# Performance work log

Measured on AMD Instinct MI355X. Metric: run time of the kernel, lower is better.

## Reference

```python
import jax, jax.numpy as jnp
import numpy as np

IN_F, HID_F, OUT_F = 2048, 8192, 2048
BATCH = 4096

def setup_inputs() -> dict:
    key = jax.random.key(0)
    k_x, k_w1, k_b1, k_w2, k_b2 = jax.random.split(key, 5)
    # PyTorch Linear default init: U(-1/sqrt(fan_in), 1/sqrt(fan_in))
    s1 = 1.0 / np.sqrt(IN_F)
    s2 = 1.0 / np.sqrt(HID_F)
    return {
        "x":  jax.random.normal(k_x, (BATCH, IN_F), dtype=jnp.float32),
        "W1": jax.random.uniform(k_w1, (IN_F, HID_F), jnp.float32, -s1, s1),
        "b1": jax.random.uniform(k_b1, (HID_F,), jnp.float32, -s1, s1),
        "W2": jax.random.uniform(k_w2, (HID_F, OUT_F), jnp.float32, -s2, s2),
        "b2": jax.random.uniform(k_b2, (OUT_F,), jnp.float32, -s2, s2),
    }

def reference(x, W1, b1, W2, b2):
    # linear1 -> ReLU -> linear2 -> sigmoid (the original's numpy "black box"
    # is mathematically 1/(1+exp(-x)), done here on-device).
    h = jax.nn.relu(x @ W1 + b1)          # [B, hidden]
    z = h @ W2 + b2                        # [B, out]
    return jax.nn.sigmoid(z)
```

## Files before the change

kernel.cpp:

```cpp
#include <hip/hip_runtime.h>
#include <hip/hip_bf16.h>
#include <stdint.h>

#define IN_F  2048
#define HID_F 8192
#define OUT_F 2048
#define BATCH 4096

typedef __attribute__((ext_vector_type(8))) short bf16x8;
typedef __attribute__((ext_vector_type(4))) float f32x4;
typedef __attribute__((ext_vector_type(8))) unsigned short u16x8;

__device__ __forceinline__ unsigned short f32_to_bf16(float f) {
  union { float f; uint32_t u; } v; v.f = f;
  uint32_t u = v.u;
  uint32_t r = u + 0x7FFF + ((u >> 16) & 1);
  return (unsigned short)(r >> 16);
}

__device__ __forceinline__ void stage16(const unsigned short* g, unsigned short* l) {
  __builtin_amdgcn_global_load_lds(
      (const __attribute__((address_space(1))) void*)g,
      (__attribute__((address_space(3))) void*)l, 16, 0, 0);
}


__global__ void cvt_f32_bf16(const float* __restrict__ in, unsigned short* __restrict__ out, int n4) {
  int i = blockIdx.x * blockDim.x + threadIdx.x;
  int stride = gridDim.x * blockDim.x;
  for (int idx = i; idx < n4; idx += stride) {
    float4 v = ((const float4*)in)[idx];
    ushort4 o;
    o.x = f32_to_bf16(v.x); o.y = f32_to_bf16(v.y);
    o.z = f32_to_bf16(v.z); o.w = f32_to_bf16(v.w);
    ((ushort4*)out)[idx] = o;
  }
}

__global__ void transpose_cvt(const float* __restrict__ in, unsigned short* __restrict__ out,
                              int R, int C) {
  __shared__ unsigned short t[64][72];
  const int tid = threadIdx.x;
  const int r0 = blockIdx.y * 64;
  const int c0 = blockIdx.x * 64;
  #pragma unroll
  for (int p = 0; p < 4; ++p) {
    int f4  = p * 256 + tid;
    int row = f4 >> 4;
    int c   = (f4 & 15) * 4;
    float4 v = *(const float4*)&in[(size_t)(r0 + row) * C + c0 + c];
    t[c + 0][row] = f32_to_bf16(v.x);
    t[c + 1][row] = f32_to_bf16(v.y);
    t[c + 2][row] = f32_to_bf16(v.z);
    t[c + 3][row] = f32_to_bf16(v.w);
  }
  __syncthreads();
  #pragma unroll
  for (int p = 0; p < 2; ++p) {
    int u  = p * 256 + tid;
    int cc = u >> 3;
    int rr = (u & 7) * 8;
    *(u16x8*)&out[(size_t)(c0 + cc) * R + r0 + rr] = *(const u16x8*)&t[cc][rr];
  }
}

template <int EPI>
__global__ __launch_bounds__(512, 2)
void gemm_bt(const unsigned short* __restrict__ A, const unsigned short* __restrict__ Bt,
             const float* __restrict__ bias, void* __restrict__ C,
             int M, int N, int K) {
  __shared__ unsigned short lA[3][128 * 64];
  __shared__ unsigned short lB[3][256 * 64];

  const int tid  = threadIdx.x;
  const int lane = tid & 63;
  const int wave = tid >> 6;
  const int wr = wave >> 2;
  const int wc = wave & 3;

  const int nbx = N >> 8;
  const int nwg = (M >> 7) * nbx;
  int wg = blockIdx.x;
  wg = (wg & 7) * (nwg >> 3) + (wg >> 3);
  const int brow = wg / nbx;
  const int bcol = wg % nbx;

  const int srow = tid >> 3;
  const int w8   = (tid & 7) * 8;
  const unsigned short* gA[2];
  const unsigned short* gB[4];
  #pragma unroll
  for (int c = 0; c < 2; ++c) {
    int row = c * 64 + srow;
    gA[c] = A + (size_t)(brow * 128 + row) * K + (w8 ^ ((row & 7) << 3));
  }
  #pragma unroll
  for (int c = 0; c < 4; ++c) {
    int row = c * 64 + srow;
    gB[c] = Bt + (size_t)(bcol * 256 + row) * K + (w8 ^ ((row & 7) << 3));
  }
  const int ldst = tid * 8;

  const int ktiles = K >> 6;

  #pragma unroll
  for (int c = 0; c < 2; ++c) stage16(gA[c],      &lA[0][c * 4096 + ldst]);
  #pragma unroll
  for (int c = 0; c < 4; ++c) stage16(gB[c],      &lB[0][c * 4096 + ldst]);
  #pragma unroll
  for (int c = 0; c < 2; ++c) stage16(gA[c] + 64, &lA[1][c * 4096 + ldst]);
  #pragma unroll
  for (int c = 0; c < 4; ++c) stage16(gB[c] + 64, &lB[1][c * 4096 + ldst]);
  #pragma unroll
  for (int c = 0; c < 2; ++c) gA[c] += 128;
  #pragma unroll
  for (int c = 0; c < 4; ++c) gB[c] += 128;

  asm volatile("s_waitcnt vmcnt(6)" ::: "memory");
  __builtin_amdgcn_s_barrier();

  f32x4 acc[4][4] = {};
  const int fr = lane & 15;
  const int fk = (lane >> 4) * 8;

  int slot = 0;
  for (int jt = 0; jt < ktiles; ++jt) {
    const int nslot = (slot + 2 >= 3) ? slot - 1 : slot + 2;
    const bool pf = (jt + 2 < ktiles);

    #pragma unroll
    for (int kk = 0; kk < 2; ++kk) {
      bf16x8 af[4], bf[4];
      #pragma unroll
      for (int m = 0; m < 4; ++m) {
        int row = wr * 64 + m * 16 + fr;
        af[m] = *(const bf16x8*)&lA[slot][row * 64 + ((kk * 32 + fk) ^ ((row & 7) << 3))];
      }
      #pragma unroll
      for (int n = 0; n < 4; ++n) {
        int row = wc * 64 + n * 16 + fr;
        bf[n] = *(const bf16x8*)&lB[slot][row * 64 + ((kk * 32 + fk) ^ ((row & 7) << 3))];
      }
      if (pf) {
        if (kk == 0) {
          stage16(gA[0], &lA[nslot][0 * 4096 + ldst]);
          stage16(gA[1], &lA[nslot][1 * 4096 + ldst]);
          stage16(gB[0], &lB[nslot][0 * 4096 + ldst]);
        } else {
          stage16(gB[1], &lB[nslot][1 * 4096 + ldst]);
          stage16(gB[2], &lB[nslot][2 * 4096 + ldst]);
          stage16(gB[3], &lB[nslot][3 * 4096 + ldst]);
        }
      }
      __builtin_amdgcn_s_barrier();
      asm volatile("s_waitcnt lgkmcnt(0)" ::: "memory");
      __builtin_amdgcn_s_setprio(1);
      #pragma unroll
      for (int m = 0; m < 4; ++m)
        #pragma unroll
        for (int n = 0; n < 4; ++n)
          acc[m][n] = __builtin_amdgcn_mfma_f32_16x16x32_bf16(af[m], bf[n], acc[m][n], 0, 0, 0);
      __builtin_amdgcn_s_setprio(0);
      __builtin_amdgcn_s_barrier();
    }

    if (pf) {
      #pragma unroll
      for (int c = 0; c < 2; ++c) gA[c] += 64;
      #pragma unroll
      for (int c = 0; c < 4; ++c) gB[c] += 64;
    }
    if (jt + 1 < ktiles) {
      if (pf) asm volatile("s_waitcnt vmcnt(6)" ::: "memory");
      else    asm volatile("s_waitcnt vmcnt(0)" ::: "memory");
      __builtin_amdgcn_s_barrier();
    }
    slot = (slot + 1 >= 3) ? 0 : slot + 1;
  }

  const int crow0 = brow * 128 + wr * 64 + (lane >> 4) * 4;
  const int ccol0 = bcol * 256 + wc * 64 + fr;
  #pragma unroll
  for (int n = 0; n < 4; ++n) {
    const int col = ccol0 + n * 16;
    const float bv = bias[col];
    #pragma unroll
    for (int m = 0; m < 4; ++m) {
      #pragma unroll
      for (int i = 0; i < 4; ++i) {
        const size_t idx = (size_t)(crow0 + m * 16 + i) * N + col;
        float v = acc[m][n][i] + bv;
        if (EPI == 0) {
          v = v > 0.f ? v : 0.f;
          ((unsigned short*)C)[idx] = f32_to_bf16(v);
        } else {
          ((float*)C)[idx] = 1.f / (1.f + __expf(-v));
        }
      }
    }
  }
}


extern "C" void kernel_launch(void* const* d_in, const int* in_sizes, int n_in,
                              void* d_out, int out_size, void* d_ws, size_t ws_size,
                              hipStream_t stream) {
  const float* x  = (const float*)d_in[0];
  const float* W1 = (const float*)d_in[1];
  const float* b1 = (const float*)d_in[2];
  const float* W2 = (const float*)d_in[3];
  const float* b2 = (const float*)d_in[4];
  float* out = (float*)d_out;

  char* ws = (char*)d_ws;
  const size_t MB = 1024 * 1024;
  unsigned short* x_bf = (unsigned short*)(ws);
  unsigned short* W1t  = (unsigned short*)(ws + 16 * MB);
  unsigned short* W2t  = (unsigned short*)(ws + 48 * MB);
  unsigned short* h_bf = (unsigned short*)(ws + 80 * MB);

  cvt_f32_bf16<<<2048, 256, 0, stream>>>(x, x_bf, (BATCH * IN_F) / 4);
  transpose_cvt<<<dim3(HID_F / 64, IN_F / 64), 256, 0, stream>>>(W1, W1t, IN_F, HID_F);
  transpose_cvt<<<dim3(OUT_F / 64, HID_F / 64), 256, 0, stream>>>(W2, W2t, HID_F, OUT_F);

  gemm_bt<0><<<(BATCH / 128) * (HID_F / 256), 512, 0, stream>>>(
      x_bf, W1t, b1, h_bf, BATCH, HID_F, IN_F);
  gemm_bt<1><<<(BATCH / 128) * (OUT_F / 256), 512, 0, stream>>>(
      h_bf, W2t, b2, out, BATCH, OUT_F, HID_F);
}
```

Measured before the change: 511.0 us.

## Switch to 256x256 GEMM tiles with split-K second GEMM and fused weight transposes

Replaces the 128x256 triple-buffered GEMM with a 256x256 tile kernel. It uses double-buffered LDS halves, with loads interleaved between MFMA phases. The second GEMM is split along K into two bf16 partial buffers, then reduced by a new kernel that adds bias and applies sigmoid. The two weight transposes are merged into one launch. The larger tile is meant to raise arithmetic intensity and split-K is meant to keep the grid large enough. The cost is an extra reduction pass, bf16 rounding of the partial sums, and more register pressure.

New measurement: 557.1 us. +9.0%, slower.

```diff
diff --git a/kernel.cpp b/kernel.cpp
--- a/kernel.cpp
+++ b/kernel.cpp
@@ -16,6 +16,10 @@
   uint32_t u = v.u;
   uint32_t r = u + 0x7FFF + ((u >> 16) & 1);
   return (unsigned short)(r >> 16);
+}
+
+__device__ __forceinline__ float bf16_to_f32(unsigned short u) {
+  union { uint32_t u; float f; } v; v.u = ((uint32_t)u) << 16; return v.f;
 }
 
 __device__ __forceinline__ void stage16(const unsigned short* g, unsigned short* l) {
@@ -37,12 +41,15 @@
   }
 }
 
-__global__ void transpose_cvt(const float* __restrict__ in, unsigned short* __restrict__ out,
-                              int R, int C) {
+__global__ void transpose2(const float* __restrict__ W1, unsigned short* __restrict__ W1t,
+                           const float* __restrict__ W2, unsigned short* __restrict__ W2t) {
   __shared__ unsigned short t[64][72];
+  int b = blockIdx.x;
+  const float* in; unsigned short* out; int R, C, bx, by;
+  if (b < 4096) { in = W1; out = W1t; R = IN_F;  C = HID_F; bx = b & 127; by = b >> 7; }
+  else { b -= 4096; in = W2; out = W2t; R = HID_F; C = OUT_F; bx = b & 31;  by = b >> 5; }
   const int tid = threadIdx.x;
-  const int r0 = blockIdx.y * 64;
-  const int c0 = blockIdx.x * 64;
+  const int r0 = by * 64, c0 = bx * 64;
   #pragma unroll
   for (int p = 0; p < 4; ++p) {
     int f4  = p * 256 + tid;
@@ -66,11 +73,11 @@
 
 template <int EPI>
 __global__ __launch_bounds__(512, 2)
-void gemm_bt(const unsigned short* __restrict__ A, const unsigned short* __restrict__ Bt,
-             const float* __restrict__ bias, void* __restrict__ C,
-             int M, int N, int K) {
-  __shared__ unsigned short lA[3][128 * 64];
-  __shared__ unsigned short lB[3][256 * 64];
+void gemm256(const unsigned short* __restrict__ A, const unsigned short* __restrict__ Bt,
+             const float* __restrict__ bias, unsigned short* __restrict__ C,
+             int M, int N, int kstride, int ktiles, int splitk) {
+  __shared__ unsigned short lA[2][2][128 * 64];
+  __shared__ unsigned short lB[2][2][128 * 64];
 
   const int tid  = threadIdx.x;
   const int lane = tid & 63;
@@ -78,127 +85,182 @@
   const int wr = wave >> 2;
   const int wc = wave & 3;
 
-  const int nbx = N >> 8;
-  const int nwg = (M >> 7) * nbx;
+  const int nbx   = N >> 8;
+  const int tiles = (M >> 8) * nbx;
+  const int nwg   = tiles * splitk;
   int wg = blockIdx.x;
   wg = (wg & 7) * (nwg >> 3) + (wg >> 3);
-  const int brow = wg / nbx;
-  const int bcol = wg % nbx;
-
-  const int srow = tid >> 3;
-  const int w8   = (tid & 7) * 8;
-  const unsigned short* gA[2];
-  const unsigned short* gB[4];
-  #pragma unroll
-  for (int c = 0; c < 2; ++c) {
-    int row = c * 64 + srow;
-    gA[c] = A + (size_t)(brow * 128 + row) * K + (w8 ^ ((row & 7) << 3));
-  }
-  #pragma unroll
-  for (int c = 0; c < 4; ++c) {
-    int row = c * 64 + srow;
-    gB[c] = Bt + (size_t)(bcol * 256 + row) * K + (w8 ^ ((row & 7) << 3));
-  }
-  const int ldst = tid * 8;
-
-  const int ktiles = K >> 6;
-
-  #pragma unroll
-  for (int c = 0; c < 2; ++c) stage16(gA[c],      &lA[0][c * 4096 + ldst]);
-  #pragma unroll
-  for (int c = 0; c < 4; ++c) stage16(gB[c],      &lB[0][c * 4096 + ldst]);
-  #pragma unroll
-  for (int c = 0; c < 2; ++c) stage16(gA[c] + 64, &lA[1][c * 4096 + ldst]);
-  #pragma unroll
-  for (int c = 0; c < 4; ++c) stage16(gB[c] + 64, &lB[1][c * 4096 + ldst]);
-  #pragma unroll
-  for (int c = 0; c < 2; ++c) gA[c] += 128;
-  #pragma unroll
-  for (int c = 0; c < 4; ++c) gB[c] += 128;
-
-  asm volatile("s_waitcnt vmcnt(6)" ::: "memory");
+  const int s    = wg / tiles;
+  const int tt   = wg - s * tiles;
+  const int brow = tt / nbx;
+  const int bcol = tt % nbx;
+  const int k0   = s * (ktiles * 64);
+
+  const unsigned short* Abase = A  + (size_t)(brow * 256) * kstride + k0;
+  const unsigned short* Bbase = Bt + (size_t)(bcol * 256) * kstride + k0;
+  int offA[2][2], offB[2][2];
+  #pragma unroll
+  for (int h = 0; h < 2; ++h)
+    #pragma unroll
+    for (int j = 0; j < 2; ++j) {
+      int f   = j * 512 + tid;
+      int row = f >> 3;
+      int cc  = ((f & 7) * 8) ^ ((row & 7) << 3);
+      offA[h][j] = (h * 128 + row) * kstride + cc;
+      offB[h][j] = offA[h][j];
+    }
+
+#define STAGE_A(buf, h, kt)  { stage16(Abase + offA[h][0] + (kt) * 64, &lA[buf][h][(size_t)tid * 8]); \
+                               stage16(Abase + offA[h][1] + (kt) * 64, &lA[buf][h][(size_t)(512 + tid) * 8]); }
+#define STAGE_B(buf, h, kt)  { stage16(Bbase + offB[h][0] + (kt) * 64, &lB[buf][h][(size_t)tid * 8]); \
+                               stage16(Bbase + offB[h][1] + (kt) * 64, &lB[buf][h][(size_t)(512 + tid) * 8]); }
+
+  STAGE_A(0, 0, 0); STAGE_A(0, 1, 0); STAGE_B(0, 0, 0); STAGE_B(0, 1, 0);
+  STAGE_A(1, 0, 1);
+  asm volatile("s_waitcnt vmcnt(2)" ::: "memory");
   __builtin_amdgcn_s_barrier();
 
-  f32x4 acc[4][4] = {};
+  f32x4 acc[8][4] = {};
   const int fr = lane & 15;
   const int fk = (lane >> 4) * 8;
-
-  int slot = 0;
-  for (int jt = 0; jt < ktiles; ++jt) {
-    const int nslot = (slot + 2 >= 3) ? slot - 1 : slot + 2;
-    const bool pf = (jt + 2 < ktiles);
-
-    #pragma unroll
-    for (int kk = 0; kk < 2; ++kk) {
-      bf16x8 af[4], bf[4];
-      #pragma unroll
-      for (int m = 0; m < 4; ++m) {
-        int row = wr * 64 + m * 16 + fr;
-        af[m] = *(const bf16x8*)&lA[slot][row * 64 + ((kk * 32 + fk) ^ ((row & 7) << 3))];
-      }
-      #pragma unroll
-      for (int n = 0; n < 4; ++n) {
-        int row = wc * 64 + n * 16 + fr;
-        bf[n] = *(const bf16x8*)&lB[slot][row * 64 + ((kk * 32 + fk) ^ ((row & 7) << 3))];
-      }
-      if (pf) {
-        if (kk == 0) {
-          stage16(gA[0], &lA[nslot][0 * 4096 + ldst]);
-          stage16(gA[1], &lA[nslot][1 * 4096 + ldst]);
-          stage16(gB[0], &lB[nslot][0 * 4096 + ldst]);
-        } else {
-          stage16(gB[1], &lB[nslot][1 * 4096 + ldst]);
-          stage16(gB[2], &lB[nslot][2 * 4096 + ldst]);
-          stage16(gB[3], &lB[nslot][3 * 4096 + ldst]);
-        }
-      }
-      __builtin_amdgcn_s_barrier();
-      asm volatile("s_waitcnt lgkmcnt(0)" ::: "memory");
-      __builtin_amdgcn_s_setprio(1);
-      #pragma unroll
-      for (int m = 0; m < 4; ++m)
-        #pragma unroll
-        for (int n = 0; n < 4; ++n)
-          acc[m][n] = __builtin_amdgcn_mfma_f32_16x16x32_bf16(af[m], bf[n], acc[m][n], 0, 0, 0);
-      __builtin_amdgcn_s_setprio(0);
-      __builtin_amdgcn_s_barrier();
+  const int bh = wc >> 1;
+  const int br0 = (wc & 1) * 64;
+
+  bf16x8 af[4][2], bf0[2][2], bf1[2][2];
+
+  for (int tau = 0; tau < ktiles; ++tau) {
+    const int buf = tau & 1, nbuf = buf ^ 1;
+    const bool st1 = (tau + 1 < ktiles);
+
+    if (st1) STAGE_A(nbuf, 1, tau + 1);
+    #pragma unroll
+    for (int m = 0; m < 4; ++m)
+      #pragma unroll
+      for (int kk = 0; kk < 2; ++kk) {
+        int row = m * 16 + fr;
+        af[m][kk] = *(const bf16x8*)&lA[buf][wr][row * 64 + ((kk * 32 + fk) ^ ((row & 7) << 3))];
+      }
+    #pragma unroll
+    for (int n = 0; n < 2; ++n)
+      #pragma unroll
+      for (int kk = 0; kk < 2; ++kk) {
+        int row = br0 + n * 16 + fr;
+        bf0[n][kk] = *(const bf16x8*)&lB[buf][bh][row * 64 + ((kk * 32 + fk) ^ ((row & 7) << 3))];
+      }
+    asm volatile("s_waitcnt lgkmcnt(8)" ::: "memory");
+    __builtin_amdgcn_s_barrier();
+    asm volatile("s_waitcnt lgkmcnt(0)" ::: "memory");
+    __builtin_amdgcn_s_setprio(1);
+    #pragma unroll
+    for (int kk = 0; kk < 2; ++kk)
+      #pragma unroll
+      for (int m = 0; m < 4; ++m)
+        #pragma unroll
+        for (int n = 0; n < 2; ++n)
+          acc[m][n] = __builtin_amdgcn_mfma_f32_16x16x32_bf16(af[m][kk], bf0[n][kk], acc[m][n], 0, 0, 0);
+    __builtin_amdgcn_s_setprio(0);
+    __builtin_amdgcn_s_barrier();
+
+    if (st1) STAGE_B(nbuf, 0, tau + 1);
+    #pragma unroll
+    for (int n = 0; n < 2; ++n)
+      #pragma unroll
+      for (int kk = 0; kk < 2; ++kk) {
+        int row = br0 + (2 + n) * 16 + fr;
+        bf1[n][kk] = *(const bf16x8*)&lB[buf][bh][row * 64 + ((kk * 32 + fk) ^ ((row & 7) << 3))];
+      }
+    __builtin_amdgcn_s_barrier();
+    asm volatile("s_waitcnt lgkmcnt(0)" ::: "memory");
+    __builtin_amdgcn_s_setprio(1);
+    #pragma unroll
+    for (int kk = 0; kk < 2; ++kk)
+      #pragma unroll
+      for (int m = 0; m < 4; ++m)
+        #pragma unroll
+        for (int n = 0; n < 2; ++n)
+          acc[m][2 + n] = __builtin_amdgcn_mfma_f32_16x16x32_bf16(af[m][kk], bf1[n][kk], acc[m][2 + n], 0, 0, 0);
+    __builtin_amdgcn_s_setprio(0);
+    __builtin_amdgcn_s_barrier();
+
+    if (st1) STAGE_B(nbuf, 1, tau + 1);
+    #pragma unroll
+    for (int m = 0; m < 4; ++m)
+      #pragma unroll
+      for (int kk = 0; kk < 2; ++kk) {
+        int row = (4 + m) * 16 + fr;
+        af[m][kk] = *(const bf16x8*)&lA[buf][wr][row * 64 + ((kk * 32 + fk) ^ ((row & 7) << 3))];
+      }
+    __builtin_amdgcn_s_barrier();
+    asm volatile("s_waitcnt lgkmcnt(0)" ::: "memory");
+    __builtin_amdgcn_s_setprio(1);
+    #pragma unroll
+    for (int kk = 0; kk < 2; ++kk)
+      #pragma unroll
+      for (int m = 0; m < 4; ++m)
+        #pragma unroll
+        for (int n = 0; n < 2; ++n)
+          acc[4 + m][2 + n] = __builtin_amdgcn_mfma_f32_16x16x32_bf16(af[m][kk], bf1[n][kk], acc[4 + m][2 + n], 0, 0, 0);
+    __builtin_amdgcn_s_setprio(0);
+    __builtin_amdgcn_s_barrier();
+
+    if (tau + 2 < ktiles) {
+      STAGE_A(buf, 0, tau + 2);
+      asm volatile("s_waitcnt vmcnt(2)" ::: "memory");
+    } else {
+      asm volatile("s_waitcnt vmcnt(0)" ::: "memory");
     }
-
-    if (pf) {
-      #pragma unroll
-      for (int c = 0; c < 2; ++c) gA[c] += 64;
-      #pragma unroll
-      for (int c = 0; c < 4; ++c) gB[c] += 64;
-    }
-    if (jt + 1 < ktiles) {
-      if (pf) asm volatile("s_waitcnt vmcnt(6)" ::: "memory");
-      else    asm volatile("s_waitcnt vmcnt(0)" ::: "memory");
-      __builtin_amdgcn_s_barrier();
-    }
-    slot = (slot + 1 >= 3) ? 0 : slot + 1;
-  }
-
-  const int crow0 = brow * 128 + wr * 64 + (lane >> 4) * 4;
+    __builtin_amdgcn_s_barrier();
+    __builtin_amdgcn_s_setprio(1);
+    #pragma unroll
+    for (int kk = 0; kk < 2; ++kk)
+      #pragma unroll
+      for (int m = 0; m < 4; ++m)
+        #pragma unroll
+        for (int n = 0; n < 2; ++n)
+          acc[4 + m][n] = __builtin_amdgcn_mfma_f32_16x16x32_bf16(af[m][kk], bf0[n][kk], acc[4 + m][n], 0, 0, 0);
+    __builtin_amdgcn_s_setprio(0);
+  }
+
+  unsigned short* Cs = C + (size_t)s * M * N;
+  const int crow0 = brow * 256 + wr * 128 + (lane >> 4) * 4;
   const int ccol0 = bcol * 256 + wc * 64 + fr;
   #pragma unroll
   for (int n = 0; n < 4; ++n) {
     const int col = ccol0 + n * 16;
-    const float bv = bias[col];
-    #pragma unroll
-    for (int m = 0; m < 4; ++m) {
+    const float bv = (EPI == 0) ? bias[col] : 0.f;
+    #pragma unroll
+    for (int m = 0; m < 8; ++m) {
       #pragma unroll
       for (int i = 0; i < 4; ++i) {
         const size_t idx = (size_t)(crow0 + m * 16 + i) * N + col;
-        float v = acc[m][n][i] + bv;
-        if (EPI == 0) {
-          v = v > 0.f ? v : 0.f;
-          ((unsigned short*)C)[idx] = f32_to_bf16(v);
-        } else {
-          ((float*)C)[idx] = 1.f / (1.f + __expf(-v));
-        }
+        float v = acc[m][n][i];
+        if (EPI == 0) { v += bv; v = v > 0.f ? v : 0.f; }
+        Cs[idx] = f32_to_bf16(v);
       }
     }
   }
+#undef STAGE_A
+#undef STAGE_B
+}
+
+__global__ void reduce_sigmoid(const unsigned short* __restrict__ p,
+                               const float* __restrict__ b2, float* __restrict__ out) {
+  const size_t i = (size_t)blockIdx.x * blockDim.x + threadIdx.x;
+  const size_t base = i * 8;
+  const int col = (int)(base & (OUT_F - 1));
+  u16x8 a = *(const u16x8*)&p[base];
+  u16x8 b = *(const u16x8*)&p[(size_t)BATCH * OUT_F + base];
+  float4 o0, o1;
+  float* o = (float*)&o0;
+  #pragma unroll
+  for (int j = 0; j < 8; ++j) {
+    float z = bf16_to_f32(a[j]) + bf16_to_f32(b[j]) + b2[col + j];
+    float r = 1.f / (1.f + __expf(-z));
+    if (j < 4) ((float*)&o0)[j] = r; else ((float*)&o1)[j - 4] = r;
+  }
+  (void)o;
+  *(float4*)&out[base] = o0;
+  *(float4*)&out[base + 4] = o1;
 }
 
 
@@ -214,17 +276,20 @@
 
   char* ws = (char*)d_ws;
   const size_t MB = 1024 * 1024;
-  unsigned short* x_bf = (unsigned short*)(ws);
-  unsigned short* W1t  = (unsigned short*)(ws + 16 * MB);
-  unsigned short* W2t  = (unsigned short*)(ws + 48 * MB);
-  unsigned short* h_bf = (unsigned short*)(ws + 80 * MB);
-
-  cvt_f32_bf16<<<2048, 256, 0, stream>>>(x, x_bf, (BATCH * IN_F) / 4);
-  transpose_cvt<<<dim3(HID_F / 64, IN_F / 64), 256, 0, stream>>>(W1, W1t, IN_F, HID_F);
-  transpose_cvt<<<dim3(OUT_F / 64, HID_F / 64), 256, 0, stream>>>(W2, W2t, HID_F, OUT_F);
-
-  gemm_bt<0><<<(BATCH / 128) * (HID_F / 256), 512, 0, stream>>>(
-      x_bf, W1t, b1, h_bf, BATCH, HID_F, IN_F);
-  gemm_bt<1><<<(BATCH / 128) * (OUT_F / 256), 512, 0, stream>>>(
-      h_bf, W2t, b2, out, BATCH, OUT_F, HID_F);
-}
+  unsigned short* x_bf  = (unsigned short*)(ws);
+  unsigned short* W1t   = (unsigned short*)(ws + 16 * MB);
+  unsigned short* W2t   = (unsigned short*)(ws + 48 * MB);
+  unsigned short* h_bf  = (unsigned short*)(ws + 80 * MB);
+  unsigned short* parts = (unsigned short*)(ws);
+
+  cvt_f32_bf16<<<4096, 256, 0, stream>>>(x, x_bf, (BATCH * IN_F) / 4);
+  transpose2<<<8192, 256, 0, stream>>>(W1, W1t, W2, W2t);
+
+  gemm256<0><<<(BATCH / 256) * (HID_F / 256), 512, 0, stream>>>(
+      x_bf, W1t, b1, h_bf, BATCH, HID_F, IN_F, IN_F / 64, 1);
+
+  gemm256<2><<<(BATCH / 256) * (OUT_F / 256) * 2, 512, 0, stream>>>(
+      h_bf, W2t, nullptr, parts, BATCH, OUT_F, HID_F, (HID_F / 2) / 64, 2);
+
+  reduce_sigmoid<<<(BATCH * OUT_F) / 8 / 256, 256, 0, stream>>>(parts, b2, out);
+}
```
